# Performance work log

Measured on AMD Instinct MI355X. Metric: run time of the kernel, lower is better.

The kernel has to match this reference:

```python
import jax, jax.numpy as jnp
import numpy as np

TOP_K = 2
SCALING = 2.0  # LoRA alpha/rank scaling


def setup_inputs() -> dict:
    key = jax.random.key(0)
    ks = jax.random.split(key, 10)
    B, S, H, I, E, R = 1, 512, 2048, 1024, 8, 16
    w = 1.0 / np.sqrt(H)
    inp = {
        "x": jax.random.normal(ks[0], (B, S, H), jnp.float32),
        "gate_weight": jax.random.normal(ks[1], (E, H), jnp.float32) * w,
        "gate_lora_A": jax.random.normal(ks[2], (R, H), jnp.float32) * 0.02,
        "gate_lora_B": jax.random.normal(ks[3], (E, R), jnp.float32) * 0.02,
        "gate_up_proj": jax.random.normal(ks[4], (E, H, 2 * I), jnp.float32) * w,
        "down_proj": jax.random.normal(ks[5], (E, I, H), jnp.float32) * (1.0 / np.sqrt(I)),
        "gup_lora_A": jax.random.normal(ks[6], (E, R, H), jnp.float32) * 0.02,
        "gup_lora_B": jax.random.normal(ks[7], (E, 2 * I, R), jnp.float32) * 0.02,
        "down_lora_A": jax.random.normal(ks[8], (E, R, I), jnp.float32) * 0.02,
        "down_lora_B": jax.random.normal(ks[9], (E, H, R), jnp.float32) * 0.02,
    }
    return inp


def reference(x, gate_weight, gate_lora_A, gate_lora_B, gate_up_proj, down_proj,
              gup_lora_A, gup_lora_B, down_lora_A, down_lora_B):
    B, S, H = x.shape
    xf = x.reshape(-1, H)  # [T, H]

    # ---- router (base weight + LoRA delta) ----
    gate_delta = SCALING * (gate_lora_B @ gate_lora_A)  # [E, H]
    router_logits = xf @ gate_weight.T + xf @ gate_delta.T  # [T, E]
    probs = jax.nn.softmax(router_logits.astype(jnp.float32), axis=-1)
    routing_weights, selected = jax.lax.top_k(probs, TOP_K)  # [T, K]
    routing_weights = routing_weights / routing_weights.sum(-1, keepdims=True)  # norm_topk_prob
    routing_weights = routing_weights.astype(xf.dtype)

    # ---- expert MLP: compute all experts, combine top-k ----
    # (math identical to sparse scatter/grouped-GEMM dispatch for selected experts)
    gup = jnp.einsum('th,eho->teo', xf, gate_up_proj)  # [T, E, 2I]
    gup = gup + SCALING * jnp.einsum('ter,eor->teo',
                                     jnp.einsum('th,erh->ter', xf, gup_lora_A),
                                     gup_lora_B)
    gates, h = jnp.split(gup, 2, axis=-1)
    h = jax.nn.silu(gates) * h  # [T, E, I]

    out = jnp.einsum('tei,eih->teh', h, down_proj)  # [T, E, H]
    out = out + SCALING * jnp.einsum('ter,ehr->teh',
                                     jnp.einsum('tei,eri->ter', h, down_lora_A),
                                     down_lora_B)

    # gather the top-k expert outputs and combine with routing weights
    out_sel = jnp.take_along_axis(out, selected[:, :, None], axis=1)  # [T, K, H]
    y = jnp.einsum('tkh,tk->th', out_sel, routing_weights)
    return y.reshape(B, S, H)
```

## Files before the change

kernel.cpp:

```cpp
#include <hip/hip_runtime.h>


typedef short  s16x8 __attribute__((ext_vector_type(8)));
typedef float  f32x4 __attribute__((ext_vector_type(4)));
typedef unsigned short u16x8 __attribute__((ext_vector_type(8)));

__device__ __forceinline__ unsigned short f2bf(float f) {
  unsigned u = __builtin_bit_cast(unsigned, f);
  u += 0x7fffu + ((u >> 16) & 1u);
  return (unsigned short)(u >> 16);
}

#define PIPE_BARRIER() asm volatile("s_waitcnt lgkmcnt(0)\n\ts_barrier" ::: "memory")

#define OFF_CNT    0u
#define OFF_TER1A  256u
#define OFF_TER2   262400u
#define ZERO_SPAN  327936u
#define OFF_LIST   327936u
#define OFF_PW     344320u
#define OFF_WG     348416u
#define OFF_XBF    413952u
#define OFF_H      2511104u

__global__ void k_gatecomb(const float* __restrict__ gw, const float* __restrict__ gA,
                           const float* __restrict__ gB, float* __restrict__ Wg) {
  int idx = blockIdx.x * 256 + threadIdx.x;
  int e = idx >> 11, h = idx & 2047;
  float acc = gw[idx];
#pragma unroll
  for (int r = 0; r < 16; ++r)
    acc += 2.0f * gB[e * 16 + r] * gA[r * 2048 + h];
  Wg[idx] = acc;
}

__global__ void k_router(const float* __restrict__ x, const float* __restrict__ Wg,
                         int* __restrict__ cnt, int* __restrict__ list,
                         float* __restrict__ pw, unsigned short* __restrict__ xbf) {
  int t = blockIdx.x, tid = threadIdx.x;
  __shared__ float xs[2048];
  __shared__ float logits[8];
  for (int i = tid; i < 2048; i += 256) xs[i] = x[(size_t)t * 2048 + i];
  __syncthreads();
  {
    u16x8 o;
#pragma unroll
    for (int j = 0; j < 8; ++j) o[j] = f2bf(xs[tid * 8 + j]);
    *(u16x8*)(xbf + (size_t)t * 2048 + tid * 8) = o;
  }
  int e = tid >> 5, l = tid & 31;
  float s = 0.f;
  for (int h = l; h < 2048; h += 32) s += xs[h] * Wg[e * 2048 + h];
#pragma unroll
  for (int off = 16; off >= 1; off >>= 1) s += __shfl_down(s, off, 32);
  if (l == 0) logits[e] = s;
  __syncthreads();
  if (tid == 0) {
    float m = logits[0];
#pragma unroll
    for (int i = 1; i < 8; ++i) m = fmaxf(m, logits[i]);
    float ex[8];
#pragma unroll
    for (int i = 0; i < 8; ++i) ex[i] = __expf(logits[i] - m);
    int e1 = 0; float v1 = ex[0];
#pragma unroll
    for (int i = 1; i < 8; ++i) if (ex[i] > v1) { v1 = ex[i]; e1 = i; }
    int e2 = -1; float v2 = -1.f;
#pragma unroll
    for (int i = 0; i < 8; ++i) if (i != e1 && ex[i] > v2) { v2 = ex[i]; e2 = i; }
    float inv = 1.f / (v1 + v2);
    int p1 = 2 * t, p2 = 2 * t + 1;
    pw[p1] = v1 * inv;
    pw[p2] = v2 * inv;
    int s1 = atomicAdd(&cnt[e1], 1); list[e1 * 512 + s1] = p1;
    int s2 = atomicAdd(&cnt[e2], 1); list[e2 * 512 + s2] = p2;
  }
}

__global__ __launch_bounds__(512) void k_ter1all(
    const unsigned short* __restrict__ xbf, const float* __restrict__ gupA,
    float* __restrict__ ter1all) {
  int trow = blockIdx.x, kcc = blockIdx.y;
  int tid = threadIdx.x;
  __shared__ unsigned short Ap[2][64 * 64];
  __shared__ unsigned short Bp[2][128 * 64];
  const int k0b = kcc * 512;

  int rowA = tid >> 3, k16A = tid & 7;
  const unsigned short* aSrc = xbf + (size_t)(trow * 64 + rowA) * 2048 + k0b + k16A * 8;
  int aOff = rowA * 64 + ((k16A * 8) ^ ((rowA & 7) << 3));

  const float* bSrc[2]; int bOff[2];
#pragma unroll
  for (int s = 0; s < 2; ++s) {
    int slot = tid + s * 512;
    int er = slot >> 3, kg = slot & 7;
    bSrc[s] = gupA + (size_t)er * 2048 + k0b + kg * 8;
    bOff[s] = er * 64 + ((kg * 8) ^ ((er & 7) << 3));
  }
  int lane = tid & 63, wv = tid >> 6;
  int lr = lane & 15, lh = lane >> 4;

  uint4 apre; float4 bpre[2][2];
#define TA_ISSUE(T) { int kk = (T) * 64;                                   \
    apre = *(const uint4*)(aSrc + kk);                                     \
    _Pragma("unroll") for (int s = 0; s < 2; ++s) {                        \
      bpre[s][0] = *(const float4*)(bSrc[s] + kk);                         \
      bpre[s][1] = *(const float4*)(bSrc[s] + kk + 4); } }

  f32x4 acc[4] = {};
  TA_ISSUE(0);
  for (int t = 0; t < 8; ++t) {
    int buf = t & 1;
    *(uint4*)&Ap[buf][aOff] = apre;
#pragma unroll
    for (int s = 0; s < 2; ++s) {
      u16x8 o;
      o[0]=f2bf(bpre[s][0].x); o[1]=f2bf(bpre[s][0].y); o[2]=f2bf(bpre[s][0].z); o[3]=f2bf(bpre[s][0].w);
      o[4]=f2bf(bpre[s][1].x); o[5]=f2bf(bpre[s][1].y); o[6]=f2bf(bpre[s][1].z); o[7]=f2bf(bpre[s][1].w);
      *(u16x8*)&Bp[buf][bOff[s]] = o;
    }
    __syncthreads();
    if (t < 7) TA_ISSUE(t + 1);
#pragma unroll
    for (int ks = 0; ks < 64; ks += 32) {
      int kb = ks + lh * 8;
      int bc = wv * 16 + lr;
      s16x8 b = *(const s16x8*)&Bp[buf][bc * 64 + (kb ^ ((bc & 7) << 3))];
#pragma unroll
      for (int fr = 0; fr < 4; ++fr) {
        int ar = fr * 16 + lr;
        s16x8 a = *(const s16x8*)&Ap[buf][ar * 64 + (kb ^ ((ar & 7) << 3))];
        acc[fr] = __builtin_amdgcn_mfma_f32_16x16x32_bf16(a, b, acc[fr], 0, 0, 0);
      }
    }
    __syncthreads();
  }
#undef TA_ISSUE
#pragma unroll
  for (int fr = 0; fr < 4; ++fr)
#pragma unroll
    for (int j = 0; j < 4; ++j) {
      int tok = trow * 64 + fr * 16 + lh * 4 + j;
      atomicAdd(&ter1all[tok * 128 + wv * 16 + lr], acc[fr][j]);
    }
}

__global__ __launch_bounds__(512) void k_gemm1(
    const unsigned short* __restrict__ xbf, const float* __restrict__ gup,
    const float* __restrict__ gupB, const float* __restrict__ ter1all,
    const int* __restrict__ cnt, const int* __restrict__ list,
    unsigned short* __restrict__ h) {
  const int id = blockIdx.x;
  const int e  = id & 7;
  const int m  = id >> 3;
  const int ct = m & 15;
  const int st = m >> 4;
  const int n = cnt[e];
  if (st * 128 >= n) return;
  const int tid = threadIdx.x;

  __shared__ unsigned short Ap[2][128 * 64];
  __shared__ unsigned short Bp[2][128 * 64];

  const int c0 = ct * 64;

  const unsigned short *aSrc0, *aSrc1;
  int aOff0, aOff1;
  {
    int row = tid >> 3, k16 = tid & 7;
    int p = list[e * 512 + min(st * 128 + row, n - 1)];
    aSrc0 = xbf + (size_t)(p >> 1) * 2048 + k16 * 8;
    aOff0 = row * 64 + ((k16 * 8) ^ ((row & 7) << 3));
    int slot = tid + 512;
    row = slot >> 3; k16 = slot & 7;
    p = list[e * 512 + min(st * 128 + row, n - 1)];
    aSrc1 = xbf + (size_t)(p >> 1) * 2048 + k16 * 8;
    aOff1 = row * 64 + ((k16 * 8) ^ ((row & 7) << 3));
  }
  const int bcol = tid & 127, kgrp = tid >> 7;
  const int gcg = (bcol < 64) ? (c0 + bcol) : (1024 + c0 + bcol - 64);
  const float* bSrc = gup + (size_t)e * 2048 * 2048 + (size_t)(kgrp * 16) * 2048 + gcg;
  const int sw = (bcol & 7) << 3;
  const int bOff0 = bcol * 64 + ((kgrp * 16) ^ sw);
  const int bOff1 = bcol * 64 + ((kgrp * 16 + 8) ^ sw);

  const int lane = tid & 63, wv = tid >> 6;
  const int lr = lane & 15, lh = lane >> 4;
  const int wr = wv >> 1, ni = wv & 1;

  uint4 a0A, a1A, a0B, a1B, a0C, a1C;
  float bA[16], bB[16], bC[16];

#define G1_LOAD(SUF, T) {                                        \
    const int kk = (T) * 64;                                     \
    a0##SUF = *(const uint4*)(aSrc0 + kk);                       \
    a1##SUF = *(const uint4*)(aSrc1 + kk);                       \
    _Pragma("unroll") for (int j = 0; j < 16; ++j)               \
      b##SUF[j] = bSrc[(size_t)(kk + j) * 2048]; }

#define G1_BODY(BUF, SUF, NXT) {                                               \
    *(uint4*)&Ap[BUF][aOff0] = a0##SUF;                                        \
    *(uint4*)&Ap[BUF][aOff1] = a1##SUF;                                        \
    { u16x8 o0, o1;                                                            \
      _Pragma("unroll") for (int j = 0; j < 8; ++j) {                          \
        o0[j] = f2bf(b##SUF[j]); o1[j] = f2bf(b##SUF[j + 8]); }                \
      *(u16x8*)&Bp[BUF][bOff0] = o0;                                           \
      *(u16x8*)&Bp[BUF][bOff1] = o1; }                                         \
    PIPE_BARRIER();                                                            \
    if ((NXT) < 32) G1_LOAD(SUF, NXT);                                         \
    _Pragma("unroll") for (int ks = 0; ks < 64; ks += 32) {                    \
      int kb = ks + lh * 8;                                                    \
      s16x8 af[2], bg[2], bu[2];                                               \
      _Pragma("unroll") for (int q = 0; q < 2; ++q) {                          \
        int ar = wr * 32 + q * 16 + lr;                                        \
        af[q] = *(const s16x8*)&Ap[BUF][ar * 64 + (kb ^ ((ar & 7) << 3))];     \
      }                                                                        \
      _Pragma("unroll") for (int r = 0; r < 2; ++r) {                          \
        int bc = ni * 32 + r * 16 + lr;                                        \
        bg[r] = *(const s16x8*)&Bp[BUF][bc * 64 + (kb ^ ((bc & 7) << 3))];     \
        bu[r] = *(const s16x8*)&Bp[BUF][(bc + 64) * 64 + (kb ^ ((bc & 7) << 3))]; \
      }                                                                        \
      _Pragma("unroll") for (int q = 0; q < 2; ++q)                            \
        _Pragma("unroll") for (int r = 0; r < 2; ++r) {                        \
          accg[q][r] = __builtin_amdgcn_mfma_f32_16x16x32_bf16(af[q], bg[r], accg[q][r], 0, 0, 0); \
          accu[q][r] = __builtin_amdgcn_mfma_f32_16x16x32_bf16(af[q], bu[r], accu[q][r], 0, 0, 0); \
        }                                                                      \
    } }

  f32x4 accg[2][2] = {}, accu[2][2] = {};
  G1_LOAD(A, 0);
  G1_LOAD(B, 1);
  G1_LOAD(C, 2);
  for (int tt = 0; tt < 30; tt += 6) {
    G1_BODY(0, A, tt + 3);
    G1_BODY(1, B, tt + 4);
    G1_BODY(0, C, tt + 5);
    G1_BODY(1, A, tt + 6);
    G1_BODY(0, B, tt + 7);
    G1_BODY(1, C, tt + 8);
  }
  G1_BODY(0, A, 99);
  G1_BODY(1, B, 99);
#undef G1_LOAD
#undef G1_BODY

  __syncthreads();
  float* tlds = (float*)&Ap[0][0];
  for (int idx = tid; idx < 2048; idx += 512) {
    int row = idx >> 4, c = idx & 15;
    int p = list[e * 512 + min(st * 128 + row, n - 1)];
    tlds[idx] = ter1all[(size_t)(p >> 1) * 128 + e * 16 + c];
  }
  __syncthreads();
#pragma unroll
  for (int r = 0; r < 2; ++r) {
    int gc = c0 + ni * 32 + r * 16 + lr;
    const float4* g4 = (const float4*)(gupB + ((size_t)e * 2048 + gc) * 16);
    const float4* u4 = (const float4*)(gupB + ((size_t)e * 2048 + 1024 + gc) * 16);
    float gv2[16], uv2[16];
#pragma unroll
    for (int q = 0; q < 4; ++q) {
      float4 gv = g4[q], uv = u4[q];
      gv2[q*4+0]=gv.x; gv2[q*4+1]=gv.y; gv2[q*4+2]=gv.z; gv2[q*4+3]=gv.w;
      uv2[q*4+0]=uv.x; uv2[q*4+1]=uv.y; uv2[q*4+2]=uv.z; uv2[q*4+3]=uv.w;
    }
#pragma unroll
    for (int q = 0; q < 2; ++q) {
#pragma unroll
      for (int j = 0; j < 4; ++j) {
        int row = wr * 32 + q * 16 + lh * 4 + j;
        if (st * 128 + row < n) {
          int p = list[e * 512 + st * 128 + row];
          const float* tv = &tlds[row * 16];
          float dg = 0.f, du = 0.f;
#pragma unroll
          for (int rr = 0; rr < 16; ++rr) { dg += tv[rr] * gv2[rr]; du += tv[rr] * uv2[rr]; }
          float g = accg[q][r][j] + 2.f * dg;
          float u = accu[q][r][j] + 2.f * du;
          h[(size_t)p * 1024 + gc] = f2bf(g / (1.f + __expf(-g)) * u);
        }
      }
    }
  }
}

__global__ __launch_bounds__(512) void k_ter2(
    const unsigned short* __restrict__ h, const float* __restrict__ dlA,
    const int* __restrict__ cnt, const int* __restrict__ list,
    float* __restrict__ ter2) {
  int st = blockIdx.x, kcc = blockIdx.y, e = blockIdx.z;
  int n = cnt[e];
  if (st * 128 >= n) return;
  int tid = threadIdx.x;
  __shared__ unsigned short Ap[2][128 * 64];
  __shared__ unsigned short Bp[2][16 * 64];
  const int k0b = kcc * 256;

  const unsigned short* aSrc[2]; int aOff[2];
#pragma unroll
  for (int s = 0; s < 2; ++s) {
    int slot = tid + s * 512;
    int row = slot >> 3, k16 = slot & 7;
    int p = list[e * 512 + min(st * 128 + row, n - 1)];
    aSrc[s] = h + (size_t)p * 1024 + k0b + k16 * 8;
    aOff[s] = row * 64 + ((k16 * 8) ^ ((row & 7) << 3));
  }
  const float* bSrc = nullptr; int bOff = 0;
  if (tid < 128) {
    int r = tid >> 3, kg = tid & 7;
    bSrc = dlA + ((size_t)e * 16 + r) * 1024 + k0b + kg * 8;
    bOff = r * 64 + ((kg * 8) ^ ((r & 7) << 3));
  }
  int lane = tid & 63, wv = tid >> 6;
  int lr = lane & 15, lh = lane >> 4;

  uint4 apre[2]; float4 bpre[2];
#define T2_ISSUE(T) { int kk = (T) * 64;                                   \
    _Pragma("unroll") for (int s = 0; s < 2; ++s)                          \
        apre[s] = *(const uint4*)(aSrc[s] + kk);                           \
    if (tid < 128) { bpre[0] = *(const float4*)(bSrc + kk);                \
                     bpre[1] = *(const float4*)(bSrc + kk + 4); } }

  f32x4 acc = {};
  T2_ISSUE(0);
  for (int t = 0; t < 4; ++t) {
    int buf = t & 1;
#pragma unroll
    for (int s = 0; s < 2; ++s) *(uint4*)&Ap[buf][aOff[s]] = apre[s];
    if (tid < 128) {
      u16x8 o;
      o[0]=f2bf(bpre[0].x); o[1]=f2bf(bpre[0].y); o[2]=f2bf(bpre[0].z); o[3]=f2bf(bpre[0].w);
      o[4]=f2bf(bpre[1].x); o[5]=f2bf(bpre[1].y); o[6]=f2bf(bpre[1].z); o[7]=f2bf(bpre[1].w);
      *(u16x8*)&Bp[buf][bOff] = o;
    }
    __syncthreads();
    if (t < 3) T2_ISSUE(t + 1);
#pragma unroll
    for (int ks = 0; ks < 64; ks += 32) {
      int kb = ks + lh * 8;
      s16x8 b = *(const s16x8*)&Bp[buf][lr * 64 + (kb ^ ((lr & 7) << 3))];
      int ar = wv * 16 + lr;
      s16x8 a = *(const s16x8*)&Ap[buf][ar * 64 + (kb ^ ((ar & 7) << 3))];
      acc = __builtin_amdgcn_mfma_f32_16x16x32_bf16(a, b, acc, 0, 0, 0);
    }
    __syncthreads();
  }
#undef T2_ISSUE
#pragma unroll
  for (int j = 0; j < 4; ++j) {
    int row = wv * 16 + lh * 4 + j;
    if (st * 128 + row < n) {
      int p = list[e * 512 + st * 128 + row];
      atomicAdd(&ter2[p * 16 + lr], acc[j]);
    }
  }
}

__global__ __launch_bounds__(512) void k_gemm2(
    const unsigned short* __restrict__ h, const float* __restrict__ down,
    const float* __restrict__ dlB, const float* __restrict__ ter2,
    const int* __restrict__ cnt, const int* __restrict__ list,
    const float* __restrict__ pw, float* __restrict__ y) {
  const int id = blockIdx.x;
  const int e  = id & 7;
  const int m  = id >> 3;
  const int ct = m & 31;
  const int st = m >> 5;
  const int n = cnt[e];
  if (st * 128 >= n) return;
  const int tid = threadIdx.x;

  __shared__ unsigned short Ap[2][128 * 64];
  __shared__ unsigned short Bp[2][64 * 64];

  const int c0 = ct * 64;

  const unsigned short *aSrc0, *aSrc1;
  int aOff0, aOff1;
  {
    int row = tid >> 3, k16 = tid & 7;
    int p = list[e * 512 + min(st * 128 + row, n - 1)];
    aSrc0 = h + (size_t)p * 1024 + k16 * 8;
    aOff0 = row * 64 + ((k16 * 8) ^ ((row & 7) << 3));
    int slot = tid + 512;
    row = slot >> 3; k16 = slot & 7;
    p = list[e * 512 + min(st * 128 + row, n - 1)];
    aSrc1 = h + (size_t)p * 1024 + k16 * 8;
    aOff1 = row * 64 + ((k16 * 8) ^ ((row & 7) << 3));
  }
  const int bcol = tid & 63, kg = tid >> 6;
  const float* bSrc = down + (size_t)e * 1024 * 2048 + (size_t)(kg * 8) * 2048 + c0 + bcol;
  const int bOff = bcol * 64 + ((kg * 8) ^ ((bcol & 7) << 3));

  const int lane = tid & 63, wv = tid >> 6;
  const int lr = lane & 15, lh = lane >> 4;
  const int wr = wv >> 1, ni = wv & 1;

  uint4 a0A, a1A, a0B, a1B, a0C, a1C;
  float bA[8], bB[8], bC[8];

#define G2_LOAD(SUF, T) {                                        \
    const int kk = (T) * 64;                                     \
    a0##SUF = *(const uint4*)(aSrc0 + kk);                       \
    a1##SUF = *(const uint4*)(aSrc1 + kk);                       \
    _Pragma("unroll") for (int j = 0; j < 8; ++j)                \
      b##SUF[j] = bSrc[(size_t)(kk + j) * 2048]; }

#define G2_BODY(BUF, SUF, NXT) {                                               \
    *(uint4*)&Ap[BUF][aOff0] = a0##SUF;                                        \
    *(uint4*)&Ap[BUF][aOff1] = a1##SUF;                                        \
    { u16x8 o;                                                                 \
      _Pragma("unroll") for (int j = 0; j < 8; ++j) o[j] = f2bf(b##SUF[j]);    \
      *(u16x8*)&Bp[BUF][bOff] = o; }                                           \
    PIPE_BARRIER();                                                            \
    if ((NXT) < 16) G2_LOAD(SUF, NXT);                                         \
    _Pragma("unroll") for (int ks = 0; ks < 64; ks += 32) {                    \
      int kb = ks + lh * 8;                                                    \
      s16x8 af[2], bd[2];                                                      \
      _Pragma("unroll") for (int q = 0; q < 2; ++q) {                          \
        int ar = wr * 32 + q * 16 + lr;                                        \
        af[q] = *(const s16x8*)&Ap[BUF][ar * 64 + (kb ^ ((ar & 7) << 3))];     \
      }                                                                        \
      _Pragma("unroll") for (int r = 0; r < 2; ++r) {                          \
        int bc = ni * 32 + r * 16 + lr;                                        \
        bd[r] = *(const s16x8*)&Bp[BUF][bc * 64 + (kb ^ ((bc & 7) << 3))];     \
      }                                                                        \
      _Pragma("unroll") for (int q = 0; q < 2; ++q)                            \
        _Pragma("unroll") for (int r = 0; r < 2; ++r)                          \
          acc[q][r] = __builtin_amdgcn_mfma_f32_16x16x32_bf16(af[q], bd[r], acc[q][r], 0, 0, 0); \
    } }

  f32x4 acc[2][2] = {};
  G2_LOAD(A, 0);
  G2_LOAD(B, 1);
  G2_LOAD(C, 2);
  for (int tt = 0; tt < 12; tt += 6) {
    G2_BODY(0, A, tt + 3);
    G2_BODY(1, B, tt + 4);
    G2_BODY(0, C, tt + 5);
    G2_BODY(1, A, tt + 6);
    G2_BODY(0, B, tt + 7);
    G2_BODY(1, C, tt + 8);
  }
  G2_BODY(0, A, 15);
  G2_BODY(1, B, 99);
  G2_BODY(0, C, 99);
  G2_BODY(1, A, 99);
#undef G2_LOAD
#undef G2_BODY

  __syncthreads();
  float* t2l = (float*)&Ap[0][0];
  for (int idx = tid; idx < 2048; idx += 512) {
    int row = idx >> 4, c = idx & 15;
    int p = list[e * 512 + min(st * 128 + row, n - 1)];
    t2l[idx] = ter2[p * 16 + c];
  }
  __syncthreads();
#pragma unroll
  for (int r = 0; r < 2; ++r) {
    int yc = c0 + ni * 32 + r * 16 + lr;
    const float4* d4 = (const float4*)(dlB + ((size_t)e * 2048 + yc) * 16);
    float d2[16];
#pragma unroll
    for (int q = 0; q < 4; ++q) {
      float4 v = d4[q];
      d2[q*4+0]=v.x; d2[q*4+1]=v.y; d2[q*4+2]=v.z; d2[q*4+3]=v.w;
    }
#pragma unroll
    for (int q = 0; q < 2; ++q) {
#pragma unroll
      for (int j = 0; j < 4; ++j) {
        int row = wr * 32 + q * 16 + lh * 4 + j;
        if (st * 128 + row < n) {
          int p = list[e * 512 + st * 128 + row];
          const float* tv = &t2l[row * 16];
          float dd = 0.f;
#pragma unroll
          for (int rr = 0; rr < 16; ++rr) dd += tv[rr] * d2[rr];
          atomicAdd(&y[(size_t)(p >> 1) * 2048 + yc],
                    pw[p] * (acc[q][r][j] + 2.f * dd));
        }
      }
    }
  }
}

extern "C" void kernel_launch(void* const* d_in, const int* in_sizes, int n_in,
                              void* d_out, int out_size, void* d_ws, size_t ws_size,
                              hipStream_t stream) {
  (void)in_sizes; (void)n_in; (void)ws_size;
  const float* x    = (const float*)d_in[0];
  const float* gw   = (const float*)d_in[1];
  const float* gA   = (const float*)d_in[2];
  const float* gB   = (const float*)d_in[3];
  const float* gup  = (const float*)d_in[4];
  const float* down = (const float*)d_in[5];
  const float* gupA = (const float*)d_in[6];
  const float* gupB = (const float*)d_in[7];
  const float* dlA  = (const float*)d_in[8];
  const float* dlB  = (const float*)d_in[9];
  float* y = (float*)d_out;

  char* w = (char*)d_ws;
  int*   cnt           = (int*)(w + OFF_CNT);
  float* ter1all       = (float*)(w + OFF_TER1A);
  float* ter2          = (float*)(w + OFF_TER2);
  int*   list          = (int*)(w + OFF_LIST);
  float* pw            = (float*)(w + OFF_PW);
  float* Wg            = (float*)(w + OFF_WG);
  unsigned short* xbf  = (unsigned short*)(w + OFF_XBF);
  unsigned short* hbuf = (unsigned short*)(w + OFF_H);

  hipMemsetAsync(w, 0, ZERO_SPAN, stream);
  hipMemsetAsync(y, 0, (size_t)out_size * sizeof(float), stream);

  k_gatecomb<<<64, 256, 0, stream>>>(gw, gA, gB, Wg);
  k_router<<<512, 256, 0, stream>>>(x, Wg, cnt, list, pw, xbf);
  k_ter1all<<<dim3(8, 4), 512, 0, stream>>>(xbf, gupA, ter1all);
  k_gemm1<<<512, 512, 0, stream>>>(xbf, gup, gupB, ter1all, cnt, list, hbuf);
  k_ter2<<<dim3(4, 4, 8), 512, 0, stream>>>(hbuf, dlA, cnt, list, ter2);
  k_gemm2<<<1024, 512, 0, stream>>>(hbuf, down, dlB, ter2, cnt, list, pw, y);
}
```

Before: 128.8 us.

## Fuse LoRA-A projections into expert GEMM main loops, drop separate kernels

Removes the k_ter1all and k_ter2 kernels and instead computes the low-rank x·A^T (and h·A^T) products inside the gemm1/gemm2 main loops. Each loop iteration stages a 16x64 bf16 tile of the LoRA-A matrix in an extra shared buffer and adds one MFMA per row fragment. This eliminates two launches, their atomics and the workspace round trip, and shrinks the zeroed span. In exchange, every column tile block recomputes the same rank-16 product redundantly, adding loads, conversions and LDS use per iteration.

Result: faster. 124.5 us (-3.3%).

```diff
diff --git a/kernel.cpp b/kernel.cpp
--- a/kernel.cpp
+++ b/kernel.cpp
@@ -14,14 +14,12 @@
 #define PIPE_BARRIER() asm volatile("s_waitcnt lgkmcnt(0)\n\ts_barrier" ::: "memory")
 
 #define OFF_CNT    0u
-#define OFF_TER1A  256u
-#define OFF_TER2   262400u
-#define ZERO_SPAN  327936u
-#define OFF_LIST   327936u
-#define OFF_PW     344320u
-#define OFF_WG     348416u
-#define OFF_XBF    413952u
-#define OFF_H      2511104u
+#define ZERO_SPAN  256u
+#define OFF_LIST   256u
+#define OFF_PW     16640u
+#define OFF_WG     20736u
+#define OFF_XBF    86272u
+#define OFF_H      2183424u
 
 __global__ void k_gatecomb(const float* __restrict__ gw, const float* __restrict__ gA,
                            const float* __restrict__ gB, float* __restrict__ Wg) {
@@ -77,78 +75,9 @@
   }
 }
 
-__global__ __launch_bounds__(512) void k_ter1all(
-    const unsigned short* __restrict__ xbf, const float* __restrict__ gupA,
-    float* __restrict__ ter1all) {
-  int trow = blockIdx.x, kcc = blockIdx.y;
-  int tid = threadIdx.x;
-  __shared__ unsigned short Ap[2][64 * 64];
-  __shared__ unsigned short Bp[2][128 * 64];
-  const int k0b = kcc * 512;
-
-  int rowA = tid >> 3, k16A = tid & 7;
-  const unsigned short* aSrc = xbf + (size_t)(trow * 64 + rowA) * 2048 + k0b + k16A * 8;
-  int aOff = rowA * 64 + ((k16A * 8) ^ ((rowA & 7) << 3));
-
-  const float* bSrc[2]; int bOff[2];
-#pragma unroll
-  for (int s = 0; s < 2; ++s) {
-    int slot = tid + s * 512;
-    int er = slot >> 3, kg = slot & 7;
-    bSrc[s] = gupA + (size_t)er * 2048 + k0b + kg * 8;
-    bOff[s] = er * 64 + ((kg * 8) ^ ((er & 7) << 3));
-  }
-  int lane = tid & 63, wv = tid >> 6;
-  int lr = lane & 15, lh = lane >> 4;
-
-  uint4 apre; float4 bpre[2][2];
-#define TA_ISSUE(T) { int kk = (T) * 64;                                   \
-    apre = *(const uint4*)(aSrc + kk);                                     \
-    _Pragma("unroll") for (int s = 0; s < 2; ++s) {                        \
-      bpre[s][0] = *(const float4*)(bSrc[s] + kk);                         \
-      bpre[s][1] = *(const float4*)(bSrc[s] + kk + 4); } }
-
-  f32x4 acc[4] = {};
-  TA_ISSUE(0);
-  for (int t = 0; t < 8; ++t) {
-    int buf = t & 1;
-    *(uint4*)&Ap[buf][aOff] = apre;
-#pragma unroll
-    for (int s = 0; s < 2; ++s) {
-      u16x8 o;
-      o[0]=f2bf(bpre[s][0].x); o[1]=f2bf(bpre[s][0].y); o[2]=f2bf(bpre[s][0].z); o[3]=f2bf(bpre[s][0].w);
-      o[4]=f2bf(bpre[s][1].x); o[5]=f2bf(bpre[s][1].y); o[6]=f2bf(bpre[s][1].z); o[7]=f2bf(bpre[s][1].w);
-      *(u16x8*)&Bp[buf][bOff[s]] = o;
-    }
-    __syncthreads();
-    if (t < 7) TA_ISSUE(t + 1);
-#pragma unroll
-    for (int ks = 0; ks < 64; ks += 32) {
-      int kb = ks + lh * 8;
-      int bc = wv * 16 + lr;
-      s16x8 b = *(const s16x8*)&Bp[buf][bc * 64 + (kb ^ ((bc & 7) << 3))];
-#pragma unroll
-      for (int fr = 0; fr < 4; ++fr) {
-        int ar = fr * 16 + lr;
-        s16x8 a = *(const s16x8*)&Ap[buf][ar * 64 + (kb ^ ((ar & 7) << 3))];
-        acc[fr] = __builtin_amdgcn_mfma_f32_16x16x32_bf16(a, b, acc[fr], 0, 0, 0);
-      }
-    }
-    __syncthreads();
-  }
-#undef TA_ISSUE
-#pragma unroll
-  for (int fr = 0; fr < 4; ++fr)
-#pragma unroll
-    for (int j = 0; j < 4; ++j) {
-      int tok = trow * 64 + fr * 16 + lh * 4 + j;
-      atomicAdd(&ter1all[tok * 128 + wv * 16 + lr], acc[fr][j]);
-    }
-}
-
 __global__ __launch_bounds__(512) void k_gemm1(
     const unsigned short* __restrict__ xbf, const float* __restrict__ gup,
-    const float* __restrict__ gupB, const float* __restrict__ ter1all,
+    const float* __restrict__ gupA, const float* __restrict__ gupB,
     const int* __restrict__ cnt, const int* __restrict__ list,
     unsigned short* __restrict__ h) {
   const int id = blockIdx.x;
@@ -162,6 +91,7 @@
 
   __shared__ unsigned short Ap[2][128 * 64];
   __shared__ unsigned short Bp[2][128 * 64];
+  __shared__ unsigned short Bp2[2][16 * 64];
 
   const int c0 = ct * 64;
 
@@ -185,19 +115,27 @@
   const int bOff0 = bcol * 64 + ((kgrp * 16) ^ sw);
   const int bOff1 = bcol * 64 + ((kgrp * 16 + 8) ^ sw);
 
+  const int gr = (tid >> 3) & 15, gk = tid & 7;
+  const float* gaSrc = gupA + ((size_t)e * 16 + gr) * 2048 + gk * 8;
+  const int gaOff = gr * 64 + ((gk * 8) ^ ((gr & 7) << 3));
+
   const int lane = tid & 63, wv = tid >> 6;
   const int lr = lane & 15, lh = lane >> 4;
   const int wr = wv >> 1, ni = wv & 1;
 
   uint4 a0A, a1A, a0B, a1B, a0C, a1C;
   float bA[16], bB[16], bC[16];
+  float4 g0A, g1A, g0B, g1B, g0C, g1C;
 
 #define G1_LOAD(SUF, T) {                                        \
     const int kk = (T) * 64;                                     \
     a0##SUF = *(const uint4*)(aSrc0 + kk);                       \
     a1##SUF = *(const uint4*)(aSrc1 + kk);                       \
     _Pragma("unroll") for (int j = 0; j < 16; ++j)               \
-      b##SUF[j] = bSrc[(size_t)(kk + j) * 2048]; }
+      b##SUF[j] = bSrc[(size_t)(kk + j) * 2048];                 \
+    if (tid < 128) {                                             \
+      g0##SUF = *(const float4*)(gaSrc + kk);                    \
+      g1##SUF = *(const float4*)(gaSrc + kk + 4); } }
 
 #define G1_BODY(BUF, SUF, NXT) {                                               \
     *(uint4*)&Ap[BUF][aOff0] = a0##SUF;                                        \
@@ -207,11 +145,17 @@
         o0[j] = f2bf(b##SUF[j]); o1[j] = f2bf(b##SUF[j + 8]); }                \
       *(u16x8*)&Bp[BUF][bOff0] = o0;                                           \
       *(u16x8*)&Bp[BUF][bOff1] = o1; }                                         \
+    if (tid < 128) { u16x8 og;                                                 \
+      og[0]=f2bf(g0##SUF.x); og[1]=f2bf(g0##SUF.y);                            \
+      og[2]=f2bf(g0##SUF.z); og[3]=f2bf(g0##SUF.w);                            \
+      og[4]=f2bf(g1##SUF.x); og[5]=f2bf(g1##SUF.y);                            \
+      og[6]=f2bf(g1##SUF.z); og[7]=f2bf(g1##SUF.w);                            \
+      *(u16x8*)&Bp2[BUF][gaOff] = og; }                                        \
     PIPE_BARRIER();                                                            \
     if ((NXT) < 32) G1_LOAD(SUF, NXT);                                         \
     _Pragma("unroll") for (int ks = 0; ks < 64; ks += 32) {                    \
       int kb = ks + lh * 8;                                                    \
-      s16x8 af[2], bg[2], bu[2];                                               \
+      s16x8 af[2], bg[2], bu[2], bt;                                           \
       _Pragma("unroll") for (int q = 0; q < 2; ++q) {                          \
         int ar = wr * 32 + q * 16 + lr;                                        \
         af[q] = *(const s16x8*)&Ap[BUF][ar * 64 + (kb ^ ((ar & 7) << 3))];     \
@@ -221,14 +165,18 @@
         bg[r] = *(const s16x8*)&Bp[BUF][bc * 64 + (kb ^ ((bc & 7) << 3))];     \
         bu[r] = *(const s16x8*)&Bp[BUF][(bc + 64) * 64 + (kb ^ ((bc & 7) << 3))]; \
       }                                                                        \
-      _Pragma("unroll") for (int q = 0; q < 2; ++q)                            \
+      bt = *(const s16x8*)&Bp2[BUF][lr * 64 + (kb ^ ((lr & 7) << 3))];         \
+      _Pragma("unroll") for (int q = 0; q < 2; ++q) {                          \
         _Pragma("unroll") for (int r = 0; r < 2; ++r) {                        \
           accg[q][r] = __builtin_amdgcn_mfma_f32_16x16x32_bf16(af[q], bg[r], accg[q][r], 0, 0, 0); \
           accu[q][r] = __builtin_amdgcn_mfma_f32_16x16x32_bf16(af[q], bu[r], accu[q][r], 0, 0, 0); \
         }                                                                      \
+        acct1[q] = __builtin_amdgcn_mfma_f32_16x16x32_bf16(af[q], bt, acct1[q], 0, 0, 0); \
+      }                                                                        \
     } }
 
   f32x4 accg[2][2] = {}, accu[2][2] = {};
+  f32x4 acct1[2] = {};
   G1_LOAD(A, 0);
   G1_LOAD(B, 1);
   G1_LOAD(C, 2);
@@ -247,10 +195,14 @@
 
   __syncthreads();
   float* tlds = (float*)&Ap[0][0];
-  for (int idx = tid; idx < 2048; idx += 512) {
-    int row = idx >> 4, c = idx & 15;
-    int p = list[e * 512 + min(st * 128 + row, n - 1)];
-    tlds[idx] = ter1all[(size_t)(p >> 1) * 128 + e * 16 + c];
+  if (ni == 0) {
+#pragma unroll
+    for (int q = 0; q < 2; ++q)
+#pragma unroll
+      for (int j = 0; j < 4; ++j) {
+        int row = wr * 32 + q * 16 + lh * 4 + j;
+        tlds[row * 16 + lr] = acct1[q][j];
+      }
   }
   __syncthreads();
 #pragma unroll
@@ -285,81 +237,9 @@
   }
 }
 
-__global__ __launch_bounds__(512) void k_ter2(
-    const unsigned short* __restrict__ h, const float* __restrict__ dlA,
-    const int* __restrict__ cnt, const int* __restrict__ list,
-    float* __restrict__ ter2) {
-  int st = blockIdx.x, kcc = blockIdx.y, e = blockIdx.z;
-  int n = cnt[e];
-  if (st * 128 >= n) return;
-  int tid = threadIdx.x;
-  __shared__ unsigned short Ap[2][128 * 64];
-  __shared__ unsigned short Bp[2][16 * 64];
-  const int k0b = kcc * 256;
-
-  const unsigned short* aSrc[2]; int aOff[2];
-#pragma unroll
-  for (int s = 0; s < 2; ++s) {
-    int slot = tid + s * 512;
-    int row = slot >> 3, k16 = slot & 7;
-    int p = list[e * 512 + min(st * 128 + row, n - 1)];
-    aSrc[s] = h + (size_t)p * 1024 + k0b + k16 * 8;
-    aOff[s] = row * 64 + ((k16 * 8) ^ ((row & 7) << 3));
-  }
-  const float* bSrc = nullptr; int bOff = 0;
-  if (tid < 128) {
-    int r = tid >> 3, kg = tid & 7;
-    bSrc = dlA + ((size_t)e * 16 + r) * 1024 + k0b + kg * 8;
-    bOff = r * 64 + ((kg * 8) ^ ((r & 7) << 3));
-  }
-  int lane = tid & 63, wv = tid >> 6;
-  int lr = lane & 15, lh = lane >> 4;
-
-  uint4 apre[2]; float4 bpre[2];
-#define T2_ISSUE(T) { int kk = (T) * 64;                                   \
-    _Pragma("unroll") for (int s = 0; s < 2; ++s)                          \
-        apre[s] = *(const uint4*)(aSrc[s] + kk);                           \
-    if (tid < 128) { bpre[0] = *(const float4*)(bSrc + kk);                \
-                     bpre[1] = *(const float4*)(bSrc + kk + 4); } }
-
-  f32x4 acc = {};
-  T2_ISSUE(0);
-  for (int t = 0; t < 4; ++t) {
-    int buf = t & 1;
-#pragma unroll
-    for (int s = 0; s < 2; ++s) *(uint4*)&Ap[buf][aOff[s]] = apre[s];
-    if (tid < 128) {
-      u16x8 o;
-      o[0]=f2bf(bpre[0].x); o[1]=f2bf(bpre[0].y); o[2]=f2bf(bpre[0].z); o[3]=f2bf(bpre[0].w);
-      o[4]=f2bf(bpre[1].x); o[5]=f2bf(bpre[1].y); o[6]=f2bf(bpre[1].z); o[7]=f2bf(bpre[1].w);
-      *(u16x8*)&Bp[buf][bOff] = o;
-    }
-    __syncthreads();
-    if (t < 3) T2_ISSUE(t + 1);
-#pragma unroll
-    for (int ks = 0; ks < 64; ks += 32) {
-      int kb = ks + lh * 8;
-      s16x8 b = *(const s16x8*)&Bp[buf][lr * 64 + (kb ^ ((lr & 7) << 3))];
-      int ar = wv * 16 + lr;
-      s16x8 a = *(const s16x8*)&Ap[buf][ar * 64 + (kb ^ ((ar & 7) << 3))];
-      acc = __builtin_amdgcn_mfma_f32_16x16x32_bf16(a, b, acc, 0, 0, 0);
-    }
-    __syncthreads();
-  }
-#undef T2_ISSUE
-#pragma unroll
-  for (int j = 0; j < 4; ++j) {
-    int row = wv * 16 + lh * 4 + j;
-    if (st * 128 + row < n) {
-      int p = list[e * 512 + st * 128 + row];
-      atomicAdd(&ter2[p * 16 + lr], acc[j]);
-    }
-  }
-}
-
 __global__ __launch_bounds__(512) void k_gemm2(
     const unsigned short* __restrict__ h, const float* __restrict__ down,
-    const float* __restrict__ dlB, const float* __restrict__ ter2,
+    const float* __restrict__ dlA, const float* __restrict__ dlB,
     const int* __restrict__ cnt, const int* __restrict__ list,
     const float* __restrict__ pw, float* __restrict__ y) {
   const int id = blockIdx.x;
@@ -373,6 +253,7 @@
 
   __shared__ unsigned short Ap[2][128 * 64];
   __shared__ unsigned short Bp[2][64 * 64];
+  __shared__ unsigned short Bp2[2][16 * 64];
 
   const int c0 = ct * 64;
 
@@ -393,19 +274,27 @@
   const float* bSrc = down + (size_t)e * 1024 * 2048 + (size_t)(kg * 8) * 2048 + c0 + bcol;
   const int bOff = bcol * 64 + ((kg * 8) ^ ((bcol & 7) << 3));
 
+  const int gr = (tid >> 3) & 15, gk = tid & 7;
+  const float* gaSrc = dlA + ((size_t)e * 16 + gr) * 1024 + gk * 8;
+  const int gaOff = gr * 64 + ((gk * 8) ^ ((gr & 7) << 3));
+
   const int lane = tid & 63, wv = tid >> 6;
   const int lr = lane & 15, lh = lane >> 4;
   const int wr = wv >> 1, ni = wv & 1;
 
   uint4 a0A, a1A, a0B, a1B, a0C, a1C;
   float bA[8], bB[8], bC[8];
+  float4 g0A, g1A, g0B, g1B, g0C, g1C;
 
 #define G2_LOAD(SUF, T) {                                        \
     const int kk = (T) * 64;                                     \
     a0##SUF = *(const uint4*)(aSrc0 + kk);                       \
     a1##SUF = *(const uint4*)(aSrc1 + kk);                       \
     _Pragma("unroll") for (int j = 0; j < 8; ++j)                \
-      b##SUF[j] = bSrc[(size_t)(kk + j) * 2048]; }
+      b##SUF[j] = bSrc[(size_t)(kk + j) * 2048];                 \
+    if (tid < 128) {                                             \
+      g0##SUF = *(const float4*)(gaSrc + kk);                    \
+      g1##SUF = *(const float4*)(gaSrc + kk + 4); } }
 
 #define G2_BODY(BUF, SUF, NXT) {                                               \
     *(uint4*)&Ap[BUF][aOff0] = a0##SUF;                                        \
@@ -413,11 +302,17 @@
     { u16x8 o;                                                                 \
       _Pragma("unroll") for (int j = 0; j < 8; ++j) o[j] = f2bf(b##SUF[j]);    \
       *(u16x8*)&Bp[BUF][bOff] = o; }                                           \
+    if (tid < 128) { u16x8 og;                                                 \
+      og[0]=f2bf(g0##SUF.x); og[1]=f2bf(g0##SUF.y);                            \
+      og[2]=f2bf(g0##SUF.z); og[3]=f2bf(g0##SUF.w);                            \
+      og[4]=f2bf(g1##SUF.x); og[5]=f2bf(g1##SUF.y);                            \
+      og[6]=f2bf(g1##SUF.z); og[7]=f2bf(g1##SUF.w);                            \
+      *(u16x8*)&Bp2[BUF][gaOff] = og; }                                        \
     PIPE_BARRIER();                                                            \
     if ((NXT) < 16) G2_LOAD(SUF, NXT);                                         \
     _Pragma("unroll") for (int ks = 0; ks < 64; ks += 32) {                    \
       int kb = ks + lh * 8;                                                    \
-      s16x8 af[2], bd[2];                                                      \
+      s16x8 af[2], bd[2], bt;                                                  \
       _Pragma("unroll") for (int q = 0; q < 2; ++q) {                          \
         int ar = wr * 32 + q * 16 + lr;                                        \
         af[q] = *(const s16x8*)&Ap[BUF][ar * 64 + (kb ^ ((ar & 7) << 3))];     \
@@ -426,12 +321,16 @@
         int bc = ni * 32 + r * 16 + lr;                                        \
         bd[r] = *(const s16x8*)&Bp[BUF][bc * 64 + (kb ^ ((bc & 7) << 3))];     \
       }                                                                        \
-      _Pragma("unroll") for (int q = 0; q < 2; ++q)                            \
+      bt = *(const s16x8*)&Bp2[BUF][lr * 64 + (kb ^ ((lr & 7) << 3))];         \
+      _Pragma("unroll") for (int q = 0; q < 2; ++q) {                          \
         _Pragma("unroll") for (int r = 0; r < 2; ++r)                          \
           acc[q][r] = __builtin_amdgcn_mfma_f32_16x16x32_bf16(af[q], bd[r], acc[q][r], 0, 0, 0); \
+        acct2[q] = __builtin_amdgcn_mfma_f32_16x16x32_bf16(af[q], bt, acct2[q], 0, 0, 0); \
+      }                                                                        \
     } }
 
   f32x4 acc[2][2] = {};
+  f32x4 acct2[2] = {};
   G2_LOAD(A, 0);
   G2_LOAD(B, 1);
   G2_LOAD(C, 2);
@@ -452,10 +351,14 @@
 
   __syncthreads();
   float* t2l = (float*)&Ap[0][0];
-  for (int idx = tid; idx < 2048; idx += 512) {
-    int row = idx >> 4, c = idx & 15;
-    int p = list[e * 512 + min(st * 128 + row, n - 1)];
-    t2l[idx] = ter2[p * 16 + c];
+  if (ni == 0) {
+#pragma unroll
+    for (int q = 0; q < 2; ++q)
+#pragma unroll
+      for (int j = 0; j < 4; ++j) {
+        int row = wr * 32 + q * 16 + lh * 4 + j;
+        t2l[row * 16 + lr] = acct2[q][j];
+      }
   }
   __syncthreads();
 #pragma unroll
@@ -505,8 +408,6 @@
 
   char* w = (char*)d_ws;
   int*   cnt           = (int*)(w + OFF_CNT);
-  float* ter1all       = (float*)(w + OFF_TER1A);
-  float* ter2          = (float*)(w + OFF_TER2);
   int*   list          = (int*)(w + OFF_LIST);
   float* pw            = (float*)(w + OFF_PW);
   float* Wg            = (float*)(w + OFF_WG);
@@ -518,8 +419,6 @@
 
   k_gatecomb<<<64, 256, 0, stream>>>(gw, gA, gB, Wg);
   k_router<<<512, 256, 0, stream>>>(x, Wg, cnt, list, pw, xbf);
-  k_ter1all<<<dim3(8, 4), 512, 0, stream>>>(xbf, gupA, ter1all);
-  k_gemm1<<<512, 512, 0, stream>>>(xbf, gup, gupB, ter1all, cnt, list, hbuf);
-  k_ter2<<<dim3(4, 4, 8), 512, 0, stream>>>(hbuf, dlA, cnt, list, ter2);
-  k_gemm2<<<1024, 512, 0, stream>>>(hbuf, down, dlB, ter2, cnt, list, pw, y);
-}
+  k_gemm1<<<512, 512, 0, stream>>>(xbf, gup, gupA, gupB, cnt, list, hbuf);
+  k_gemm2<<<1024, 512, 0, stream>>>(hbuf, down, dlA, dlB, cnt, list, pw, y);
+}
```
